# Kernel optimization log

Hardware: AMD Instinct MI355X
Metric: run time of the kernel (lower is better)

The kernel has to match this reference:

```python
import jax, jax.numpy as jnp
import numpy as np

# dims: batch N, queries Q, frames F, patches-per-frame L, heads H, head_dim D
N, Q, F, L, H, D = 32, 64, 16, 196, 12, 64
E = H * D          # embed_dim = 768
K = F * L          # kv length = 3136


def setup_inputs() -> dict:
    key = jax.random.key(0)
    kq, kk, kv, km, kw1, kw2 = jax.random.split(key, 6)
    q = jax.random.normal(kq, (N, Q, E), dtype=jnp.float32)
    k = jax.random.normal(kk, (N, K, H, D), dtype=jnp.float32)
    v = jax.random.normal(kv, (N, K, H, D), dtype=jnp.float32)
    # frame-padding mask; guarantee >=1 valid patch per frame so the
    # per-frame softmax never sees an all -inf group (NaN otherwise)
    m = jax.random.bernoulli(km, 0.9, (N, K))
    m = m.reshape(N, F, L).at[:, :, 0].set(True).reshape(N, K)
    W_in = jax.random.normal(kw1, (E, E), dtype=jnp.float32) * 0.02   # in_proj (n_act=1)
    W_out = jax.random.normal(kw2, (E, E), dtype=jnp.float32) * 0.02  # out_proj
    return {"q": q, "k": k, "v": v, "m": m, "W_in": W_in, "W_out": W_out}


def reference(q, k, v, m, W_in, W_out):
    n, nq, e = q.shape
    h, d = H, e // H
    # in_proj (no bias) then split into heads; n_act == 1 so qs has one element
    qs = (q @ W_in.T).reshape(n, nq, h, d)
    # scaled QK affinity: [n, Q, K, h]
    aff = jnp.einsum('nqhc,nkhc->nqkh', qs * (d ** -0.5), k)
    # frame mask broadcast over queries and heads
    aff = jnp.where(m[:, None, :, None], aff, -jnp.inf)
    kn = aff.shape[2]
    # grouped softmax over patches within each frame (dim=-2 of the view)
    aff = jax.nn.softmax(aff.reshape(n, nq, F, kn // F, h), axis=-2)
    aff = aff.reshape(n, nq, kn, h)
    # mix with v and output projection
    mix = jnp.einsum('nqlh,nlhc->nqhc', aff, v)
    out = mix.reshape(n, nq, e) @ W_out.T
    # second return: stacked flattened qs, shape [n, n_act=1, Q, E]
    qs_out = qs.reshape(n, nq, e)[:, None]
    return out, qs_out
```

## Files before the change

kernel.cpp:

```cpp
#include <hip/hip_runtime.h>
#include <hip/hip_bf16.h>
#include <cfloat>

#define N_B 32
#define QN 64
#define FN 16
#define LP 196
#define HN 12
#define DH 64
#define EE 768
#define KLEN 3136
#define FPB 4
#define KROWS 208
#define VST 232

typedef short s16x4 __attribute__((ext_vector_type(4)));
typedef __bf16 bf16x8 __attribute__((ext_vector_type(8)));
typedef float f32x4 __attribute__((ext_vector_type(4)));

__device__ __forceinline__ bf16x8 cvt8(f32x4 a, f32x4 b) {
    bf16x8 r;
    r[0] = (__bf16)a[0]; r[1] = (__bf16)a[1]; r[2] = (__bf16)a[2]; r[3] = (__bf16)a[3];
    r[4] = (__bf16)b[0]; r[5] = (__bf16)b[1]; r[6] = (__bf16)b[2]; r[7] = (__bf16)b[3];
    return r;
}
__device__ __forceinline__ unsigned short bfb(float x) {
    return __builtin_bit_cast(unsigned short, (__bf16)x);
}

__global__ __launch_bounds__(256) void gemm_mfma(const float* __restrict__ A,
                                                 const float* __restrict__ W,
                                                 float* __restrict__ C) {
    __shared__ unsigned short As[64 * 72];
    __shared__ unsigned short Ws[48 * 72];
    const int t = threadIdx.x;
    const int w = t >> 6, lane = t & 63, lr = lane & 15, lg = lane >> 4;
    const int m0 = blockIdx.x * 64;
    const int n0 = blockIdx.y * 48;

    f32x4 acc[3];
#pragma unroll
    for (int ct = 0; ct < 3; ++ct) acc[ct] = (f32x4){0.f, 0.f, 0.f, 0.f};

    for (int k0 = 0; k0 < EE; k0 += 32) {
        {
            int row = t >> 2, cb = t & 3;
            const float* src = A + (size_t)(m0 + row) * EE + k0 + cb * 8;
            f32x4 a = *(const f32x4*)src, b = *(const f32x4*)(src + 4);
            *(bf16x8*)&As[row * 72 + cb * 8] = cvt8(a, b);
        }
        if (t < 192) {
            int row = t >> 2, cb = t & 3;
            const float* src = W + (size_t)(n0 + row) * EE + k0 + cb * 8;
            f32x4 a = *(const f32x4*)src, b = *(const f32x4*)(src + 4);
            *(bf16x8*)&Ws[row * 72 + cb * 8] = cvt8(a, b);
        }
        __syncthreads();
        bf16x8 a = *(const bf16x8*)&As[(w * 16 + lr) * 72 + lg * 8];
#pragma unroll
        for (int ct = 0; ct < 3; ++ct) {
            bf16x8 b = *(const bf16x8*)&Ws[(ct * 16 + lr) * 72 + lg * 8];
            acc[ct] = __builtin_amdgcn_mfma_f32_16x16x32_bf16(a, b, acc[ct], 0, 0, 0);
        }
        __syncthreads();
    }
#pragma unroll
    for (int ct = 0; ct < 3; ++ct)
#pragma unroll
        for (int r = 0; r < 4; ++r)
            C[(size_t)(m0 + w * 16 + lg * 4 + r) * EE + n0 + ct * 16 + lr] = acc[ct][r];
}

__global__ __launch_bounds__(256) void zero_f32(float* __restrict__ p, int n4) {
    int i = blockIdx.x * 256 + threadIdx.x;
    if (i < n4) ((float4*)p)[i] = make_float4(0.f, 0.f, 0.f, 0.f);
}

__global__ __launch_bounds__(256, 2) void attn_mfma(const float* __restrict__ qs_g,
                                                    const float* __restrict__ k_g,
                                                    const float* __restrict__ v_g,
                                                    const int* __restrict__ m_g,
                                                    float* __restrict__ mix_g) {
    const int h = blockIdx.x, fg = blockIdx.y, n = blockIdx.z;

    __shared__ unsigned short KV_s[64 * VST];
    __shared__ unsigned short Pt_s[64 * VST];
    __shared__ float bias_s[224];
    __shared__ float linv_s[4][16];

    const int t = threadIdx.x;
    const int w = t >> 6, lane = t & 63, lr = lane & 15, lg = lane >> 4;

    {
        int qr = t >> 2, c0 = 208 + (t & 3) * 4;
        *(s16x4*)&Pt_s[qr * VST + c0] = (s16x4){0, 0, 0, 0};
    }
    bf16x8 qb0, qb1;
    {
        const float* qp = qs_g + ((size_t)n * QN + w * 16 + lr) * EE + h * DH + lg * 8;
        f32x4 a = *(const f32x4*)qp, b = *(const f32x4*)(qp + 4);
        f32x4 c = *(const f32x4*)(qp + 32), d = *(const f32x4*)(qp + 36);
#pragma unroll
        for (int i = 0; i < 4; ++i) { a[i] *= 0.125f; b[i] *= 0.125f; c[i] *= 0.125f; d[i] *= 0.125f; }
        qb0 = cvt8(a, b);
        qb1 = cvt8(c, d);
    }

    float mix[4][4];
#pragma unroll
    for (int dt = 0; dt < 4; ++dt)
#pragma unroll
        for (int r = 0; r < 4; ++r) mix[dt][r] = 0.f;

    for (int ff = 0; ff < FPB; ++ff) {
        const int f = fg * FPB + ff;
        const size_t kbase = (size_t)n * KLEN + f * LP;

        __syncthreads();

#pragma unroll
        for (int u = 0; u < 7; ++u) {
            int unit = t + 256 * u;
            if (unit < KROWS * 8) {
                int p = unit >> 3, blk = unit & 7;
                f32x4 a = {0.f, 0.f, 0.f, 0.f}, b = {0.f, 0.f, 0.f, 0.f};
                if (p < LP) {
                    const float* src = k_g + ((kbase + p) * HN + h) * DH + blk * 8;
                    a = *(const f32x4*)src;
                    b = *(const f32x4*)(src + 4);
                }
                *(bf16x8*)&KV_s[p * 64 + ((blk ^ (p & 7)) << 3)] = cvt8(a, b);
            }
        }
        if (t < 224) {
            float bv = -1e30f;
            if (t < LP && m_g[kbase + t] != 0) bv = 0.f;
            bias_s[t] = bv;
        }
        __syncthreads();

        f32x4 sc[13];
#pragma unroll
        for (int tl = 0; tl < 13; ++tl) {
            int row = tl * 16 + lr;
            bf16x8 a0 = *(const bf16x8*)&KV_s[row * 64 + ((lg ^ (lr & 7)) << 3)];
            bf16x8 a1 = *(const bf16x8*)&KV_s[row * 64 + (((4 + lg) ^ (lr & 7)) << 3)];
            f32x4 z = {0.f, 0.f, 0.f, 0.f};
            z = __builtin_amdgcn_mfma_f32_16x16x32_bf16(a0, qb0, z, 0, 0, 0);
            sc[tl] = __builtin_amdgcn_mfma_f32_16x16x32_bf16(a1, qb1, z, 0, 0, 0);
        }

        f32x4 va[7], vb[7];
#pragma unroll
        for (int u = 0; u < 7; ++u) {
            int unit = t + 256 * u;
            int d4 = unit / 112, pp = unit % 112;
            int p0 = pp * 2;
            va[u] = (f32x4){0.f, 0.f, 0.f, 0.f};
            vb[u] = (f32x4){0.f, 0.f, 0.f, 0.f};
            if (p0 < LP) {
                const float* vg = v_g + ((kbase + p0) * HN + h) * DH + d4 * 4;
                va[u] = *(const f32x4*)vg;
                if (p0 + 1 < LP) vb[u] = *(const f32x4*)(vg + (size_t)HN * DH);
            }
        }

        float mx = -FLT_MAX;
#pragma unroll
        for (int tl = 0; tl < 13; ++tl)
#pragma unroll
            for (int r = 0; r < 4; ++r) {
                float sv = sc[tl][r] + bias_s[tl * 16 + lg * 4 + r];
                sc[tl][r] = sv;
                mx = fmaxf(mx, sv);
            }
        mx = fmaxf(mx, __shfl_xor(mx, 16));
        mx = fmaxf(mx, __shfl_xor(mx, 32));
        float sum = 0.f;
#pragma unroll
        for (int tl = 0; tl < 13; ++tl)
#pragma unroll
            for (int r = 0; r < 4; ++r) {
                float e = __expf(sc[tl][r] - mx);
                sc[tl][r] = e;
                sum += e;
            }
        sum += __shfl_xor(sum, 16);
        sum += __shfl_xor(sum, 32);
        if (lane < 16) linv_s[w][lane] = 1.0f / sum;

#pragma unroll
        for (int tl = 0; tl < 13; ++tl) {
            s16x4 pb = {(short)bfb(sc[tl][0]), (short)bfb(sc[tl][1]),
                        (short)bfb(sc[tl][2]), (short)bfb(sc[tl][3])};
            *(s16x4*)&Pt_s[(w * 16 + lr) * VST + tl * 16 + lg * 4] = pb;
        }
        __syncthreads();

#pragma unroll
        for (int u = 0; u < 7; ++u) {
            int unit = t + 256 * u;
            int d4 = unit / 112, pp = unit % 112;
            int p0 = pp * 2;
#pragma unroll
            for (int i = 0; i < 4; ++i) {
                unsigned pk = (unsigned)bfb(va[u][i]) | ((unsigned)bfb(vb[u][i]) << 16);
                *(unsigned*)&KV_s[(d4 * 4 + i) * VST + p0] = pk;
            }
        }
        __syncthreads();

        f32x4 pv[4];
#pragma unroll
        for (int dt = 0; dt < 4; ++dt) pv[dt] = (f32x4){0.f, 0.f, 0.f, 0.f};
#pragma unroll
        for (int ks = 0; ks < 7; ++ks) {
            bf16x8 a = *(const bf16x8*)&Pt_s[(w * 16 + lr) * VST + ks * 32 + lg * 8];
#pragma unroll
            for (int dt = 0; dt < 4; ++dt) {
                bf16x8 b = *(const bf16x8*)&KV_s[(dt * 16 + lr) * VST + ks * 32 + lg * 8];
                pv[dt] = __builtin_amdgcn_mfma_f32_16x16x32_bf16(a, b, pv[dt], 0, 0, 0);
            }
        }
        float li[4];
#pragma unroll
        for (int r = 0; r < 4; ++r) li[r] = linv_s[w][lg * 4 + r];
#pragma unroll
        for (int dt = 0; dt < 4; ++dt)
#pragma unroll
            for (int r = 0; r < 4; ++r) mix[dt][r] += pv[dt][r] * li[r];
    }

#pragma unroll
    for (int dt = 0; dt < 4; ++dt)
#pragma unroll
        for (int r = 0; r < 4; ++r)
            atomicAdd(mix_g + ((size_t)n * QN + w * 16 + lg * 4 + r) * EE + h * DH + dt * 16 + lr,
                      mix[dt][r]);
}

extern "C" void kernel_launch(void* const* d_in, const int* in_sizes, int n_in,
                              void* d_out, int out_size, void* d_ws, size_t ws_size,
                              hipStream_t stream) {
    const float* q  = (const float*)d_in[0];
    const float* k  = (const float*)d_in[1];
    const float* v  = (const float*)d_in[2];
    const int*   m  = (const int*)d_in[3];
    const float* Wi = (const float*)d_in[4];
    const float* Wo = (const float*)d_in[5];

    float* out = (float*)d_out;
    float* qs  = out + (size_t)N_B * QN * EE;
    float* mix = (float*)d_ws;

    const int mix_n4 = (N_B * QN * EE) / 4;
    dim3 ggrid((N_B * QN) / 64, EE / 48);
    gemm_mfma<<<ggrid, 256, 0, stream>>>(q, Wi, qs);
    zero_f32<<<(mix_n4 + 255) / 256, 256, 0, stream>>>(mix, mix_n4);
    attn_mfma<<<dim3(HN, FN / FPB, N_B), 256, 0, stream>>>(qs, k, v, m, mix);
    gemm_mfma<<<ggrid, 256, 0, stream>>>(mix, Wo, out);
}
```

Measured before the change: 236.8 us.

## Prefetch next frame's K and mask into registers, swizzle V tile in LDS

The next frame's K rows and mask are loaded into registers while the current frame's softmax and PV run, then converted to bf16 and stored to shared memory at the start of the next iteration. This hides global-load latency behind compute. The V global load mapping now has consecutive threads read consecutive 16-byte chunks of one row, which should improve coalescing. The transposed V tile uses a 256-element stride with an XOR swizzle to cut LDS bank conflicts. The cost is many extra live registers under a two-blocks-per-SM launch bound, which risks spills or lower occupancy.

Result: slower. 410.6 us (+73.4%).

```diff
diff --git a/kernel.cpp b/kernel.cpp
--- a/kernel.cpp
+++ b/kernel.cpp
@@ -12,7 +12,8 @@
 #define KLEN 3136
 #define FPB 4
 #define KROWS 208
-#define VST 232
+#define VST 256
+#define PST 232
 
 typedef short s16x4 __attribute__((ext_vector_type(4)));
 typedef __bf16 bf16x8 __attribute__((ext_vector_type(8)));
@@ -84,7 +85,7 @@
     const int h = blockIdx.x, fg = blockIdx.y, n = blockIdx.z;
 
     __shared__ unsigned short KV_s[64 * VST];
-    __shared__ unsigned short Pt_s[64 * VST];
+    __shared__ unsigned short Pt_s[64 * PST];
     __shared__ float bias_s[224];
     __shared__ float linv_s[4][16];
 
@@ -93,7 +94,7 @@
 
     {
         int qr = t >> 2, c0 = 208 + (t & 3) * 4;
-        *(s16x4*)&Pt_s[qr * VST + c0] = (s16x4){0, 0, 0, 0};
+        *(s16x4*)&Pt_s[qr * PST + c0] = (s16x4){0, 0, 0, 0};
     }
     bf16x8 qb0, qb1;
     {
@@ -106,6 +107,25 @@
         qb1 = cvt8(c, d);
     }
 
+    bf16x8 kpre[7];
+    int mpre;
+    {
+        const size_t kb0 = (size_t)n * KLEN + (size_t)(fg * FPB) * LP;
+#pragma unroll
+        for (int u = 0; u < 7; ++u) {
+            int unit = t + 256 * u;
+            int p = unit >> 3, blk = unit & 7;
+            f32x4 a = {0.f, 0.f, 0.f, 0.f}, b = {0.f, 0.f, 0.f, 0.f};
+            if (unit < KROWS * 8 && p < LP) {
+                const float* src = k_g + ((kb0 + p) * HN + h) * DH + blk * 8;
+                a = *(const f32x4*)src;
+                b = *(const f32x4*)(src + 4);
+            }
+            kpre[u] = cvt8(a, b);
+        }
+        mpre = (t < LP) ? m_g[kb0 + t] : 0;
+    }
+
     float mix[4][4];
 #pragma unroll
     for (int dt = 0; dt < 4; ++dt)
@@ -113,8 +133,7 @@
         for (int r = 0; r < 4; ++r) mix[dt][r] = 0.f;
 
     for (int ff = 0; ff < FPB; ++ff) {
-        const int f = fg * FPB + ff;
-        const size_t kbase = (size_t)n * KLEN + f * LP;
+        const size_t kbase = (size_t)n * KLEN + (size_t)(fg * FPB + ff) * LP;
 
         __syncthreads();
 
@@ -123,20 +142,10 @@
             int unit = t + 256 * u;
             if (unit < KROWS * 8) {
                 int p = unit >> 3, blk = unit & 7;
-                f32x4 a = {0.f, 0.f, 0.f, 0.f}, b = {0.f, 0.f, 0.f, 0.f};
-                if (p < LP) {
-                    const float* src = k_g + ((kbase + p) * HN + h) * DH + blk * 8;
-                    a = *(const f32x4*)src;
-                    b = *(const f32x4*)(src + 4);
-                }
-                *(bf16x8*)&KV_s[p * 64 + ((blk ^ (p & 7)) << 3)] = cvt8(a, b);
-            }
-        }
-        if (t < 224) {
-            float bv = -1e30f;
-            if (t < LP && m_g[kbase + t] != 0) bv = 0.f;
-            bias_s[t] = bv;
-        }
+                *(bf16x8*)&KV_s[p * 64 + ((blk ^ (p & 7)) << 3)] = kpre[u];
+            }
+        }
+        if (t < 224) bias_s[t] = (t < LP && mpre != 0) ? 0.f : -1e30f;
         __syncthreads();
 
         f32x4 sc[13];
@@ -154,7 +163,7 @@
 #pragma unroll
         for (int u = 0; u < 7; ++u) {
             int unit = t + 256 * u;
-            int d4 = unit / 112, pp = unit % 112;
+            int pp = unit >> 4, d4 = unit & 15;
             int p0 = pp * 2;
             va[u] = (f32x4){0.f, 0.f, 0.f, 0.f};
             vb[u] = (f32x4){0.f, 0.f, 0.f, 0.f};
@@ -165,6 +174,24 @@
             }
         }
 
+        f32x4 ka[7], kb[7];
+        if (ff + 1 < FPB) {
+            const size_t kbn = kbase + LP;
+#pragma unroll
+            for (int u = 0; u < 7; ++u) {
+                int unit = t + 256 * u;
+                int p = unit >> 3, blk = unit & 7;
+                ka[u] = (f32x4){0.f, 0.f, 0.f, 0.f};
+                kb[u] = (f32x4){0.f, 0.f, 0.f, 0.f};
+                if (unit < KROWS * 8 && p < LP) {
+                    const float* src = k_g + ((kbn + p) * HN + h) * DH + blk * 8;
+                    ka[u] = *(const f32x4*)src;
+                    kb[u] = *(const f32x4*)(src + 4);
+                }
+            }
+            mpre = (t < LP) ? m_g[kbn + t] : 0;
+        }
+
         float mx = -FLT_MAX;
 #pragma unroll
         for (int tl = 0; tl < 13; ++tl)
@@ -193,19 +220,22 @@
         for (int tl = 0; tl < 13; ++tl) {
             s16x4 pb = {(short)bfb(sc[tl][0]), (short)bfb(sc[tl][1]),
                         (short)bfb(sc[tl][2]), (short)bfb(sc[tl][3])};
-            *(s16x4*)&Pt_s[(w * 16 + lr) * VST + tl * 16 + lg * 4] = pb;
-        }
-        __syncthreads();
-
-#pragma unroll
-        for (int u = 0; u < 7; ++u) {
-            int unit = t + 256 * u;
-            int d4 = unit / 112, pp = unit % 112;
+            *(s16x4*)&Pt_s[(w * 16 + lr) * PST + tl * 16 + lg * 4] = pb;
+        }
+        __syncthreads();
+
+#pragma unroll
+        for (int u = 0; u < 7; ++u) {
+            int unit = t + 256 * u;
+            int pp = unit >> 4, d4 = unit & 15;
             int p0 = pp * 2;
+            int blk = p0 >> 3, sub = p0 & 7;
 #pragma unroll
             for (int i = 0; i < 4; ++i) {
+                int row = d4 * 4 + i;
+                int g = (row + (row >> 2)) & 7;
                 unsigned pk = (unsigned)bfb(va[u][i]) | ((unsigned)bfb(vb[u][i]) << 16);
-                *(unsigned*)&KV_s[(d4 * 4 + i) * VST + p0] = pk;
+                *(unsigned*)&KV_s[row * VST + (((blk ^ g) << 3) | sub)] = pk;
             }
         }
         __syncthreads();
@@ -215,10 +245,12 @@
         for (int dt = 0; dt < 4; ++dt) pv[dt] = (f32x4){0.f, 0.f, 0.f, 0.f};
 #pragma unroll
         for (int ks = 0; ks < 7; ++ks) {
-            bf16x8 a = *(const bf16x8*)&Pt_s[(w * 16 + lr) * VST + ks * 32 + lg * 8];
+            bf16x8 a = *(const bf16x8*)&Pt_s[(w * 16 + lr) * PST + ks * 32 + lg * 8];
 #pragma unroll
             for (int dt = 0; dt < 4; ++dt) {
-                bf16x8 b = *(const bf16x8*)&KV_s[(dt * 16 + lr) * VST + ks * 32 + lg * 8];
+                int row = dt * 16 + lr;
+                int g = (row + (row >> 2)) & 7;
+                bf16x8 b = *(const bf16x8*)&KV_s[row * VST + (((ks * 4 + lg) ^ g) << 3)];
                 pv[dt] = __builtin_amdgcn_mfma_f32_16x16x32_bf16(a, b, pv[dt], 0, 0, 0);
             }
         }
@@ -229,6 +261,11 @@
         for (int dt = 0; dt < 4; ++dt)
 #pragma unroll
             for (int r = 0; r < 4; ++r) mix[dt][r] += pv[dt][r] * li[r];
+
+        if (ff + 1 < FPB) {
+#pragma unroll
+            for (int u = 0; u < 7; ++u) kpre[u] = cvt8(ka[u], kb[u]);
+        }
     }
 
 #pragma unroll
```
